# Optimization experiments

Hardware: AMD Instinct MI355X
Metric: run time of the kernel (lower is better)

The kernel has to match this reference:

```python
import jax, jax.numpy as jnp
import numpy as np

D_MODEL = 1024
D_STATE = 128
D_CONV = 4
EXPAND = 2
HEADDIM = 64
NGROUPS = 1
CHUNK = 256
D_INNER = EXPAND * D_MODEL          # 2048
NHEADS = D_INNER // HEADDIM         # 32
D_IN_PROJ = 2 * D_INNER + 2 * NGROUPS * D_STATE + NHEADS  # 4384
CONV_DIM = D_INNER + 2 * NGROUPS * D_STATE                # 2304
BATCH, SEQLEN = 2, 2048


def rmsnorm(x, w, eps=1e-6):
    ms = jnp.mean(x * x, axis=-1, keepdims=True)
    return w * (x * jax.lax.rsqrt(ms + eps))


def layernorm(x, eps=1e-5):
    mu = jnp.mean(x, axis=-1, keepdims=True)
    var = jnp.mean((x - mu) ** 2, axis=-1, keepdims=True)
    return (x - mu) * jax.lax.rsqrt(var + eps)


def activation_quant(x):
    # int8-style fake quant with STE, scale differentiable (matches torch)
    amax = jnp.clip(jnp.max(jnp.abs(x), axis=-1, keepdims=True), 1e-5, None)
    scale = 127.0 / amax
    q = jnp.clip(jnp.round(x * scale), -128, 127)
    return (jax.lax.stop_gradient(q - x * scale) + x * scale) / scale


def weight_quant(w):
    # ternary {-1,0,1}; note: NOT rescaled by scale (matches the triton kernel)
    scale = jnp.clip(jnp.mean(jnp.abs(w)), 1e-5, None)
    wq = jnp.clip(jnp.round(w / scale), -1.0, 1.0)
    return w + jax.lax.stop_gradient(wq - w)  # STE: identity grad


def bitlinear(x, w):
    return activation_quant(layernorm(x)) @ weight_quant(w).T


def segsum(x):
    # x: [..., T] -> [..., T, T] lower-triangular cumulative segment sums
    T = x.shape[-1]
    cs = jnp.cumsum(x, axis=-1)
    ss = cs[..., :, None] - cs[..., None, :]
    mask = jnp.tril(jnp.ones((T, T), dtype=bool))
    return jnp.where(mask, ss, -jnp.inf)


def ssd(u, a, B, C, chunk):
    # u: b l h p (= x*dt); a: b l h (= A*dt); B, C: b l h n (per-head)
    b, l, h, p = u.shape
    n = B.shape[-1]
    c = l // chunk
    u = u.reshape(b, c, chunk, h, p)
    a = a.reshape(b, c, chunk, h).transpose(0, 3, 1, 2)   # b h c s
    B = B.reshape(b, c, chunk, h, n)
    C = C.reshape(b, c, chunk, h, n)
    a_cs = jnp.cumsum(a, axis=-1)                          # b h c s
    L = jnp.exp(segsum(a))                                 # b h c s s
    Y_diag = jnp.einsum('bclhn,bcshn,bhcls,bcshp->bclhp', C, B, L, u)
    decay_states = jnp.exp(a_cs[..., -1:] - a_cs)          # b h c s
    states = jnp.einsum('bclhn,bhcl,bclhp->bchpn', B, decay_states, u)
    a_chunk = jnp.pad(a_cs[..., -1], ((0, 0), (0, 0), (1, 0)))  # b h (c+1)
    decay_chunk = jnp.exp(segsum(a_chunk))                 # b h (c+1) (c+1)
    states = jnp.concatenate([jnp.zeros_like(states[:, :1]), states], axis=1)
    new_states = jnp.einsum('bhzc,bchpn->bzhpn', decay_chunk, states)
    prev_states = new_states[:, :-1]                       # state entering each chunk
    Y_off = jnp.einsum('bclhn,bchpn,bhcl->bclhp', C, prev_states, jnp.exp(a_cs))
    return (Y_diag + Y_off).reshape(b, l, h, p)


def setup_inputs() -> dict:
    key = jax.random.key(0)
    ks = jax.random.split(key, 6)
    hidden_states = jax.random.normal(ks[0], (BATCH, SEQLEN, D_MODEL), jnp.float32)
    in_proj_w = jax.random.normal(ks[1], (D_IN_PROJ, D_MODEL), jnp.float32) / np.sqrt(D_MODEL).astype(np.float32)
    out_proj_w = jax.random.normal(ks[2], (D_MODEL, D_INNER), jnp.float32) / np.sqrt(D_INNER).astype(np.float32)
    conv_w = jax.random.normal(ks[3], (CONV_DIM, D_CONV), jnp.float32) * 0.1
    conv_b = jnp.zeros((CONV_DIM,), jnp.float32)
    A_log = jnp.log(jnp.arange(1, NHEADS + 1, dtype=jnp.float32))
    Dp = jnp.ones((NHEADS,), jnp.float32)
    dt_min, dt_max, dt_floor = 1e-3, 1e-1, 1e-4
    inv_dt = jnp.exp(jax.random.uniform(ks[4], (NHEADS,)) * (np.log(dt_max) - np.log(dt_min)) + np.log(dt_min))
    inv_dt = jnp.clip(inv_dt, dt_floor, None)
    dt_bias = inv_dt + jnp.log(-jnp.expm1(-inv_dt))
    norm_w = jnp.ones((D_MODEL,), jnp.float32)
    out_norm_w = jnp.ones((D_INNER,), jnp.float32)
    return dict(hidden_states=hidden_states, norm_w=norm_w, in_proj_w=in_proj_w,
                conv_w=conv_w, conv_b=conv_b, A_log=A_log, Dp=Dp, dt_bias=dt_bias,
                out_norm_w=out_norm_w, out_proj_w=out_proj_w)


def reference(hidden_states, norm_w, in_proj_w, conv_w, conv_b, A_log, Dp, dt_bias, out_norm_w, out_proj_w):
    b, l, _ = hidden_states.shape
    h = rmsnorm(hidden_states, norm_w)
    zxbcdt = bitlinear(h, in_proj_w)                       # b l (2*d_inner + 2*g*n + h)
    z = zxbcdt[..., :D_INNER]
    xBC = zxbcdt[..., D_INNER:D_INNER + CONV_DIM]
    dt = zxbcdt[..., D_INNER + CONV_DIM:]                  # b l h
    # causal depthwise conv1d (kernel D_CONV) + silu
    xp = jnp.pad(xBC, ((0, 0), (D_CONV - 1, 0), (0, 0)))
    conv = sum(xp[:, k:k + l, :] * conv_w[:, k] for k in range(D_CONV)) + conv_b
    xBC = jax.nn.silu(conv)
    x = xBC[..., :D_INNER].reshape(b, l, NHEADS, HEADDIM)
    Bm = xBC[..., D_INNER:D_INNER + NGROUPS * D_STATE].reshape(b, l, NGROUPS, D_STATE)
    Cm = xBC[..., D_INNER + NGROUPS * D_STATE:].reshape(b, l, NGROUPS, D_STATE)
    hpg = NHEADS // NGROUPS
    Bh = jnp.repeat(Bm, hpg, axis=2)                       # b l h n
    Ch = jnp.repeat(Cm, hpg, axis=2)
    dt = jax.nn.softplus(dt + dt_bias)                     # dt_softplus=True
    A = -jnp.exp(A_log)
    y = ssd(x * dt[..., None], dt * A, Bh, Ch, CHUNK)      # b l h p
    y = y + x * Dp[None, None, :, None]                    # D skip
    y = y * jax.nn.silu(z).reshape(b, l, NHEADS, HEADDIM)  # z gate
    y = rmsnorm(y.reshape(b, l, D_INNER), out_norm_w)
    out = bitlinear(y, out_proj_w)
    return hidden_states + out
```

## Files before the change

kernel.cpp:

```cpp
#include <hip/hip_runtime.h>
#include <stdint.h>
#include <stddef.h>
#include <math.h>

#define TOKS 4096
#define DM   1024
#define DIP  4384
#define DI   2048
#define CVD  2304
#define NH   32
#define HD   64
#define DST  128
#define NCH  8
#define CHK  256

typedef int v4i  __attribute__((ext_vector_type(4)));
typedef int v16i __attribute__((ext_vector_type(16)));
typedef short s8v __attribute__((ext_vector_type(8)));
typedef float f16v __attribute__((ext_vector_type(16)));
typedef unsigned short ushort_t;

static const size_t OFF_ZX    = 0;
static const size_t OFF_SX    = OFF_ZX + (size_t)TOKS*DIP*4;
static const size_t OFF_ST    = OFF_SX + (size_t)TOKS*CVD*4;
static const size_t OFF_YG    = OFF_ST + (size_t)512*HD*DST*4;
static const size_t OFF_Q1    = OFF_YG + (size_t)TOKS*DI*4;
static const size_t OFF_Q2    = OFF_Q1 + (size_t)TOKS*DM;
static const size_t OFF_WQ1   = OFF_Q2 + (size_t)TOKS*DI;
static const size_t OFF_WQ2   = OFF_WQ1 + (size_t)DIP*DM;
static const size_t OFF_RS1   = OFF_WQ2 + (size_t)DM*DI;
static const size_t OFF_RS2   = OFF_RS1 + (size_t)TOKS*4;
static const size_t OFF_DT    = OFF_RS2 + (size_t)TOKS*4;
static const size_t OFF_ACS   = OFF_DT + (size_t)TOKS*NH*4;
static const size_t OFF_CSUM  = OFF_ACS + (size_t)512*CHK*8;
static const size_t OFF_PART  = OFF_CSUM + 512*8;
static const size_t OFF_WSC   = OFF_PART + 1024*8;
static const size_t OFF_BH    = OFF_WSC + 64;
static const size_t OFF_BL    = OFF_BH  + (size_t)TOKS*128*2;
static const size_t OFF_CHG   = OFF_BL  + (size_t)TOKS*128*2;
static const size_t OFF_CLG   = OFF_CHG + (size_t)TOKS*128*2;
static const size_t OFF_GRAM  = OFF_CLG + (size_t)TOKS*128*2;
static const size_t OFF_UTH   = OFF_GRAM + (size_t)16*256*256*4;
static const size_t OFF_UTL   = OFF_UTH + (size_t)512*64*256*2;
static const size_t OFF_PH    = OFF_UTL + (size_t)512*64*256*2;
static const size_t OFF_PL    = OFF_PH  + (size_t)512*64*128*2;

__device__ __forceinline__ ushort_t f2bf(float x) {
  union { float f; unsigned int u; } v; v.f = x;
  unsigned int r = v.u + 0x7FFFu + ((v.u >> 16) & 1u);
  return (ushort_t)(r >> 16);
}
__device__ __forceinline__ float bf2f(ushort_t h) {
  union { unsigned int u; float f; } v; v.u = ((unsigned int)h) << 16;
  return v.f;
}

__device__ __forceinline__ double bsumd(double v, double* sb) {
#pragma unroll
  for (int o = 32; o; o >>= 1) v += __shfl_down(v, o);
  int lane = threadIdx.x & 63, w = threadIdx.x >> 6;
  __syncthreads();
  if (lane == 0) sb[w] = v;
  __syncthreads();
  return sb[0] + sb[1] + sb[2] + sb[3];
}
__device__ __forceinline__ double bmaxd(double v, double* sb) {
#pragma unroll
  for (int o = 32; o; o >>= 1) v = fmax(v, __shfl_down(v, o));
  int lane = threadIdx.x & 63, w = threadIdx.x >> 6;
  __syncthreads();
  if (lane == 0) sb[w] = v;
  __syncthreads();
  return fmax(fmax(sb[0], sb[1]), fmax(sb[2], sb[3]));
}

__global__ void __launch_bounds__(256) k_absmean(const float* __restrict__ w, int n, double* __restrict__ part) {
  double s = 0.0;
  for (int i = blockIdx.x * 256 + threadIdx.x; i < n; i += 512 * 256) s += (double)fabsf(w[i]);
  __shared__ double sb[4];
  s = bsumd(s, sb);
  if (threadIdx.x == 0) part[blockIdx.x] = s;
}

__global__ void __launch_bounds__(256) k_wscale(const double* __restrict__ part, double* __restrict__ wsc, int n1, int n2) {
  __shared__ double sb[4];
  double s = part[threadIdx.x] + part[threadIdx.x + 256];
  double t1 = bsumd(s, sb);
  __syncthreads();
  s = part[512 + threadIdx.x] + part[512 + threadIdx.x + 256];
  double t2 = bsumd(s, sb);
  if (threadIdx.x == 0) {
    wsc[0] = fmax(t1 / (double)n1, 1e-5);
    wsc[1] = fmax(t2 / (double)n2, 1e-5);
  }
}

__global__ void __launch_bounds__(256) k_tern(const float* __restrict__ w, int n, const double* __restrict__ wsc, int which, int8_t* __restrict__ out) {
  int i = blockIdx.x * 256 + threadIdx.x;
  if (i < n) {
    double sc = wsc[which];
    double q = fmin(fmax(rint((double)w[i] / sc), -1.0), 1.0);
    out[i] = (int8_t)q;
  }
}

template <int D>
__global__ void __launch_bounds__(256) k_normquant(const float* __restrict__ in, const float* __restrict__ w,
                                                   int8_t* __restrict__ q, float* __restrict__ rs) {
  constexpr int E = D / 256;
  int t = blockIdx.x, tid = threadIdx.x;
  const float* row = in + (size_t)t * D;
  __shared__ double sb[4];
  double x[E];
  double ss = 0.0;
#pragma unroll
  for (int i = 0; i < E; i++) { x[i] = (double)row[tid + 256 * i]; ss += x[i] * x[i]; }
  ss = bsumd(ss, sb);
  double rr = 1.0 / sqrt(ss / (double)D + 1e-6);
  double s1 = 0.0;
#pragma unroll
  for (int i = 0; i < E; i++) { x[i] = (double)w[tid + 256 * i] * (x[i] * rr); s1 += x[i]; }
  s1 = bsumd(s1, sb);
  double mu = s1 / (double)D;
  double s2 = 0.0;
#pragma unroll
  for (int i = 0; i < E; i++) { double d = x[i] - mu; s2 += d * d; }
  s2 = bsumd(s2, sb);
  double rv = 1.0 / sqrt(s2 / (double)D + 1e-5);
  double am = 0.0;
#pragma unroll
  for (int i = 0; i < E; i++) { x[i] = (x[i] - mu) * rv; am = fmax(am, fabs(x[i])); }
  am = bmaxd(am, sb);
  am = fmax(am, 1e-5);
  double sc = 127.0 / am;
#pragma unroll
  for (int i = 0; i < E; i++) {
    double qq = fmin(fmax(rint(x[i] * sc), -128.0), 127.0);
    q[(size_t)t * D + tid + 256 * i] = (int8_t)qq;
  }
  if (tid == 0) rs[t] = (float)(am / 127.0);
}

__global__ void __launch_bounds__(256, 3) k_gemm_mfma(const int8_t* __restrict__ A, const int8_t* __restrict__ W,
                                                      const float* __restrict__ rs, const float* __restrict__ addend,
                                                      float* __restrict__ out, int M, int N, int K) {
  __shared__ int8_t Al[128 * 80];
  __shared__ int8_t Bl[128 * 80];
  int m0 = blockIdx.x * 128, n0 = blockIdx.y * 128;
  int t = threadIdx.x;
  int w = t >> 6, lane = t & 63;
  int wm = w >> 1, wn = w & 1;
  int l31 = lane & 31, lh = lane >> 5;

  v16i acc[2][2] = {};

  for (int k0 = 0; k0 < K; k0 += 64) {
    __syncthreads();
#pragma unroll
    for (int it = 0; it < 2; ++it) {
      int c = t + 256 * it;
      int row = c >> 2, kc = (c & 3) * 16;
      int4 av = *(const int4*)(A + (size_t)(m0 + row) * K + k0 + kc);
      *(int4*)(Al + row * 80 + kc) = av;
      int4 bv;
      if (n0 + row < N) bv = *(const int4*)(W + (size_t)(n0 + row) * K + k0 + kc);
      else { bv.x = bv.y = bv.z = bv.w = 0; }
      *(int4*)(Bl + row * 80 + kc) = bv;
    }
    __syncthreads();
#pragma unroll
    for (int ks = 0; ks < 2; ++ks) {
      v4i af[2], bf[2];
#pragma unroll
      for (int tm = 0; tm < 2; ++tm)
        af[tm] = *(const v4i*)(Al + (wm * 64 + tm * 32 + l31) * 80 + ks * 32 + lh * 16);
#pragma unroll
      for (int tn = 0; tn < 2; ++tn)
        bf[tn] = *(const v4i*)(Bl + (wn * 64 + tn * 32 + l31) * 80 + ks * 32 + lh * 16);
#pragma unroll
      for (int tm = 0; tm < 2; ++tm)
#pragma unroll
        for (int tn = 0; tn < 2; ++tn)
          acc[tm][tn] = __builtin_amdgcn_mfma_i32_32x32x32_i8(af[tm], bf[tn], acc[tm][tn], 0, 0, 0);
    }
  }

#pragma unroll
  for (int tm = 0; tm < 2; ++tm)
#pragma unroll
    for (int tn = 0; tn < 2; ++tn) {
      int n = n0 + wn * 64 + tn * 32 + l31;
      if (n < N) {
#pragma unroll
        for (int r = 0; r < 16; ++r) {
          int mrel = (r & 3) + 8 * (r >> 2) + 4 * lh;
          int m = m0 + wm * 64 + tm * 32 + mrel;
          float v = rs[m] * (float)acc[tm][tn][r];
          if (addend) v += addend[(size_t)m * N + n];
          out[(size_t)m * N + n] = v;
        }
      }
    }
}

__global__ void __launch_bounds__(256) k_conv(const float* __restrict__ zx, const float* __restrict__ cw,
                                              const float* __restrict__ cb, float* __restrict__ sx) {
  int c = blockIdx.x * 256 + threadIdx.x;
  int t = blockIdx.y;
  int b = t >> 11, l = t & 2047;
  float acc = cb[c];
#pragma unroll
  for (int k = 0; k < 4; k++) {
    int li = l - 3 + k;
    if (li >= 0) acc = fmaf(zx[(size_t)(b * 2048 + li) * DIP + DI + c], cw[c * 4 + k], acc);
  }
  sx[(size_t)t * CVD + c] = acc / (1.f + expf(-acc));
}

__global__ void __launch_bounds__(256) k_splitbc(const float* __restrict__ sx,
                                                 ushort_t* __restrict__ bh, ushort_t* __restrict__ bl,
                                                 ushort_t* __restrict__ ch, ushort_t* __restrict__ cl) {
  int idx = blockIdx.x * 256 + threadIdx.x;
  int tok = idx >> 6, c4 = (idx & 63) * 4;
  float4 v = *(const float4*)(sx + (size_t)tok * CVD + DI + c4);
  float f[4] = {v.x, v.y, v.z, v.w};
  ushort_t hh[4], ll[4];
#pragma unroll
  for (int j = 0; j < 4; j++) { hh[j] = f2bf(f[j]); ll[j] = f2bf(f[j] - bf2f(hh[j])); }
  uint2 hv, lv;
  hv.x = (unsigned)hh[0] | ((unsigned)hh[1] << 16); hv.y = (unsigned)hh[2] | ((unsigned)hh[3] << 16);
  lv.x = (unsigned)ll[0] | ((unsigned)ll[1] << 16); lv.y = (unsigned)ll[2] | ((unsigned)ll[3] << 16);
  if (c4 < 128) {
    *(uint2*)(bh + (size_t)tok * 128 + c4) = hv;
    *(uint2*)(bl + (size_t)tok * 128 + c4) = lv;
  } else {
    *(uint2*)(ch + (size_t)tok * 128 + c4 - 128) = hv;
    *(uint2*)(cl + (size_t)tok * 128 + c4 - 128) = lv;
  }
}

__global__ void __launch_bounds__(256) k_dt(const float* __restrict__ zx, const float* __restrict__ dt_bias,
                                            float* __restrict__ dtv) {
  int idx = blockIdx.x * 256 + threadIdx.x;
  int t = idx >> 5, h = idx & 31;
  float x = zx[(size_t)t * DIP + (DI + CVD) + h] + dt_bias[h];
  dtv[idx] = fmaxf(x, 0.f) + log1pf(expf(-fabsf(x)));
}

__global__ void __launch_bounds__(256) k_cumsum(const float* __restrict__ dtv, const float* __restrict__ A_log,
                                                double* __restrict__ acs, double* __restrict__ csum) {
  int bid = blockIdx.x;
  int h = bid & 31, bc = bid >> 5;
  int s = threadIdx.x;
  int tok = bc * 256 + s;
  double negA = -exp((double)A_log[h]);
  double a = (double)dtv[tok * 32 + h] * negA;
  __shared__ double buf[256];
  buf[s] = a;
  __syncthreads();
  for (int o = 1; o < 256; o <<= 1) {
    double add = (s >= o) ? buf[s - o] : 0.0;
    __syncthreads();
    buf[s] += add;
    __syncthreads();
  }
  acs[(size_t)bid * 256 + s] = buf[s];
  if (s == 255) csum[bid] = buf[s];
}

__global__ void __launch_bounds__(256) k_gram(const ushort_t* __restrict__ bhg, const ushort_t* __restrict__ blg,
                                              const ushort_t* __restrict__ chg, const ushort_t* __restrict__ clg,
                                              float* __restrict__ gram) {
  int blk = blockIdx.x;
  int bc = blk >> 3, lt = blk & 7;
  int t = threadIdx.x;
  int w = t >> 6, lane = t & 63;
  int l31 = lane & 31, lhf = lane >> 5;
  __shared__ float Gl[4][32 * 36];

  s8v ch[8], cl[8];
  size_t tokA = (size_t)(bc * 256 + lt * 32 + l31) * 128;
#pragma unroll
  for (int ks = 0; ks < 8; ++ks) {
    ch[ks] = *(const s8v*)(chg + tokA + ks * 16 + lhf * 8);
    cl[ks] = *(const s8v*)(clg + tokA + ks * 16 + lhf * 8);
  }
  for (int st = w; st <= lt; st += 4) {
    size_t tokB = (size_t)(bc * 256 + st * 32 + l31) * 128;
    f16v acc = {};
#pragma unroll
    for (int ks = 0; ks < 8; ++ks) {
      s8v bh = *(const s8v*)(bhg + tokB + ks * 16 + lhf * 8);
      s8v bl = *(const s8v*)(blg + tokB + ks * 16 + lhf * 8);
      acc = __builtin_amdgcn_mfma_f32_32x32x16_bf16(ch[ks], bh, acc, 0, 0, 0);
      acc = __builtin_amdgcn_mfma_f32_32x32x16_bf16(ch[ks], bl, acc, 0, 0, 0);
      acc = __builtin_amdgcn_mfma_f32_32x32x16_bf16(cl[ks], bh, acc, 0, 0, 0);
    }
#pragma unroll
    for (int rr = 0; rr < 16; ++rr) {
      int lrow = (rr & 3) + 8 * (rr >> 2) + 4 * lhf;
      Gl[w][lrow * 36 + l31] = acc[rr];
    }
    int lr = lane >> 1, c0 = (lane & 1) * 16;
    float* gdst = gram + ((size_t)bc * 256 + lt * 32 + lr) * 256 + st * 32 + c0;
#pragma unroll
    for (int i = 0; i < 4; ++i)
      *(float4*)(gdst + i * 4) = *(const float4*)(&Gl[w][lr * 36 + c0 + i * 4]);
  }
}

__global__ void __launch_bounds__(256) k_prepuT(const float* __restrict__ sx, const float* __restrict__ dtv,
                                                ushort_t* __restrict__ uth, ushort_t* __restrict__ utl) {
  int r = blockIdx.x;
  int h = r & 31, bc = r >> 5;
  int t = threadIdx.x;
  __shared__ float Xs[64 * 68];
  __shared__ float dts[64];
  for (int slab = 0; slab < 4; ++slab) {
    int s0 = slab * 64;
    if (slab) __syncthreads();
    if (t < 64) dts[t] = dtv[(size_t)(bc * 256 + s0 + t) * 32 + h];
    {
      int s = t >> 2, pg = (t & 3) * 16;
      const float* xr = sx + (size_t)(bc * 256 + s0 + s) * CVD + h * 64 + pg;
      float* dst = &Xs[s * 68 + pg];
#pragma unroll
      for (int i = 0; i < 4; ++i)
        *(float4*)(dst + i * 4) = *(const float4*)(xr + i * 4);
    }
    __syncthreads();
    {
      int p = t >> 2, sg = (t & 3) * 16;
      union { int4 q[2]; ushort_t e[16]; } H, L;
#pragma unroll
      for (int j = 0; j < 16; ++j) {
        float f = Xs[(sg + j) * 68 + p] * dts[sg + j];
        ushort_t hh = f2bf(f);
        H.e[j] = hh;
        L.e[j] = f2bf(f - bf2f(hh));
      }
      size_t base = ((size_t)r * 64 + p) * 256 + s0 + sg;
      *(int4*)(uth + base) = H.q[0];
      *(int4*)(uth + base + 8) = H.q[1];
      *(int4*)(utl + base) = L.q[0];
      *(int4*)(utl + base + 8) = L.q[1];
    }
  }
}

__global__ void __launch_bounds__(256, 4) k_states2(const float* __restrict__ sx, const float* __restrict__ dtv,
                                                    const double* __restrict__ acs, const double* __restrict__ csum,
                                                    float* __restrict__ states) {
  int r = blockIdx.x;
  int h = r & 31, bc = r >> 5;
  int t = threadIdx.x, tx = t & 15, ty = t >> 4;
  __shared__ float du[64 * 68];
  double last = csum[r];
  float acc[4][8] = {};
  for (int s0 = 0; s0 < 256; s0 += 64) {
    __syncthreads();
    {
      int s = t >> 2, pg = (t & 3) * 16;
      int tok = bc * 256 + s0 + s;
      float w = expf((float)(last - acs[(size_t)r * 256 + s0 + s])) * dtv[(size_t)tok * 32 + h];
      const float* xr = sx + (size_t)tok * CVD + h * 64 + pg;
      float* dst = &du[s * 68 + pg];
#pragma unroll
      for (int i = 0; i < 4; i++) {
        float4 v = *(const float4*)(xr + i * 4);
        v.x *= w; v.y *= w; v.z *= w; v.w *= w;
        *(float4*)(dst + i * 4) = v;
      }
    }
    __syncthreads();
#pragma unroll 4
    for (int s = 0; s < 64; s++) {
      int tok = bc * 256 + s0 + s;
      const float* br = sx + (size_t)tok * CVD + DI + ty * 8;
      float4 b0 = *(const float4*)(br);
      float4 b1 = *(const float4*)(br + 4);
      float4 d4 = *(const float4*)(&du[s * 68 + tx * 4]);
      float dd[4] = {d4.x, d4.y, d4.z, d4.w};
      float bv[8] = {b0.x, b0.y, b0.z, b0.w, b1.x, b1.y, b1.z, b1.w};
#pragma unroll
      for (int i = 0; i < 4; i++)
#pragma unroll
        for (int j = 0; j < 8; j++) acc[i][j] = fmaf(dd[i], bv[j], acc[i][j]);
    }
  }
  size_t base = (size_t)r * (HD * DST);
#pragma unroll
  for (int i = 0; i < 4; i++) {
    float4 v0, v1;
    v0.x = acc[i][0]; v0.y = acc[i][1]; v0.z = acc[i][2]; v0.w = acc[i][3];
    v1.x = acc[i][4]; v1.y = acc[i][5]; v1.z = acc[i][6]; v1.w = acc[i][7];
    *(float4*)(states + base + (size_t)(tx * 4 + i) * DST + ty * 8) = v0;
    *(float4*)(states + base + (size_t)(tx * 4 + i) * DST + ty * 8 + 4) = v1;
  }
}

__global__ void __launch_bounds__(256) k_chunkscan(float* __restrict__ states, const double* __restrict__ csum,
                                                   ushort_t* __restrict__ ph, ushort_t* __restrict__ pl) {
  int idx = blockIdx.x * 256 + threadIdx.x;
  int n = idx & 127, p = (idx >> 7) & 63, h = (idx >> 13) & 31, b = idx >> 18;
  float Nv = 0.f;
  for (int c = 0; c < 8; c++) {
    int bid = (b * 8 + c) * 32 + h;
    size_t addr = (size_t)bid * (HD * DST) + p * DST + n;
    float s = states[addr];
    states[addr] = Nv;
    ushort_t hh = f2bf(Nv);
    ph[addr] = hh;
    pl[addr] = f2bf(Nv - bf2f(hh));
    Nv = Nv * expf((float)csum[bid]) + s;
  }
}

__global__ void __launch_bounds__(256) k_y6(const float* __restrict__ sx, const double* __restrict__ acs,
                                            const ushort_t* __restrict__ chg, const ushort_t* __restrict__ clg,
                                            const ushort_t* __restrict__ prevh, const ushort_t* __restrict__ prevl,
                                            const float* __restrict__ gram,
                                            const ushort_t* __restrict__ uth, const ushort_t* __restrict__ utl,
                                            const float* __restrict__ zx, const float* __restrict__ Dp,
                                            float* __restrict__ yg) {
  int bid = blockIdx.x;
  int r = bid >> 1, half = bid & 1;
  int h = r & 31, bc = r >> 5;
  int t = threadIdx.x;
  int w = t >> 6, lane = t & 63;
  int l31 = lane & 31, lhf = lane >> 5;
  int lw = half * 128 + w * 32;
  int lg = lw + l31;

  __shared__ ushort_t Uh[2][64 * 36], Ul[2][64 * 36];
  __shared__ double acs_s[256];
  acs_s[t] = acs[(size_t)r * 256 + t];

  int nsub = half * 4 + 4;
  {
    int p = t >> 2, sg = (t & 3) * 8;
    size_t gb = ((size_t)r * 64 + p) * 256 + sg;
    const uint2* s1 = (const uint2*)(uth + gb);
    uint2* d1 = (uint2*)(&Uh[0][p * 36 + sg]);
    d1[0] = s1[0]; d1[1] = s1[1];
    const uint2* s2 = (const uint2*)(utl + gb);
    uint2* d2 = (uint2*)(&Ul[0][p * 36 + sg]);
    d2[0] = s2[0]; d2[1] = s2[1];
  }
  __syncthreads();

  f16v Yacc[2] = {};
  {
    size_t ca = (size_t)(bc * 256 + lg) * 128;
#pragma unroll
    for (int ks = 0; ks < 8; ++ks) {
      s8v ch = *(const s8v*)(chg + ca + ks * 16 + lhf * 8);
      s8v cl = *(const s8v*)(clg + ca + ks * 16 + lhf * 8);
#pragma unroll
      for (int pt = 0; pt < 2; ++pt) {
        size_t pa = ((size_t)r * 64 + pt * 32 + l31) * 128 + ks * 16 + lhf * 8;
        s8v ph = *(const s8v*)(prevh + pa);
        s8v pl = *(const s8v*)(prevl + pa);
        Yacc[pt] = __builtin_amdgcn_mfma_f32_32x32x16_bf16(ch, ph, Yacc[pt], 0, 0, 0);
        Yacc[pt] = __builtin_amdgcn_mfma_f32_32x32x16_bf16(ch, pl, Yacc[pt], 0, 0, 0);
        Yacc[pt] = __builtin_amdgcn_mfma_f32_32x32x16_bf16(cl, ph, Yacc[pt], 0, 0, 0);
      }
    }
  }
#pragma unroll
  for (int rr = 0; rr < 16; ++rr) {
    int lrow = (rr & 3) + 8 * (rr >> 2) + 4 * lhf;
    float el = expf((float)acs_s[lw + lrow]);
    Yacc[0][rr] *= el;
    Yacc[1][rr] *= el;
  }

  for (int st = 0; st < nsub; ++st) {
    int s0 = st * 32, cur = st & 1;
    if (st + 1 < nsub) {
      int p = t >> 2, sg = (t & 3) * 8;
      int nb = cur ^ 1;
      size_t gb = ((size_t)r * 64 + p) * 256 + s0 + 32 + sg;
      const uint2* s1 = (const uint2*)(uth + gb);
      uint2* d1 = (uint2*)(&Uh[nb][p * 36 + sg]);
      d1[0] = s1[0]; d1[1] = s1[1];
      const uint2* s2 = (const uint2*)(utl + gb);
      uint2* d2 = (uint2*)(&Ul[nb][p * 36 + sg]);
      d2[0] = s2[0]; d2[1] = s2[1];
    }
    if (s0 <= lw + 31) {
      double a_l = acs_s[lg];
      const float* gp = gram + ((size_t)(bc * 256 + lg)) * 256 + s0;
#pragma unroll
      for (int ks2 = 0; ks2 < 2; ++ks2) {
        int kb = ks2 * 16 + lhf * 8;
        float4 g0 = *(const float4*)(gp + kb);
        float4 g1 = *(const float4*)(gp + kb + 4);
        float gv[8] = {g0.x, g0.y, g0.z, g0.w, g1.x, g1.y, g1.z, g1.w};
        union { s8v v; ushort_t e[8]; } AH, AL;
#pragma unroll
        for (int j = 0; j < 8; ++j) {
          int s = s0 + kb + j;
          float v = 0.f;
          if (s <= lg) v = expf((float)(a_l - acs_s[s])) * gv[j];
          ushort_t hh = f2bf(v);
          AH.e[j] = hh;
          AL.e[j] = f2bf(v - bf2f(hh));
        }
#pragma unroll
        for (int pt = 0; pt < 2; ++pt) {
          union { s8v v; uint2 d[2]; } uh, ul;
          int ub = (pt * 32 + l31) * 36 + kb;
          uh.d[0] = *(const uint2*)(&Uh[cur][ub]);
          uh.d[1] = *(const uint2*)(&Uh[cur][ub + 4]);
          ul.d[0] = *(const uint2*)(&Ul[cur][ub]);
          ul.d[1] = *(const uint2*)(&Ul[cur][ub + 4]);
          Yacc[pt] = __builtin_amdgcn_mfma_f32_32x32x16_bf16(AH.v, uh.v, Yacc[pt], 0, 0, 0);
          Yacc[pt] = __builtin_amdgcn_mfma_f32_32x32x16_bf16(AH.v, ul.v, Yacc[pt], 0, 0, 0);
          Yacc[pt] = __builtin_amdgcn_mfma_f32_32x32x16_bf16(AL.v, uh.v, Yacc[pt], 0, 0, 0);
        }
      }
    }
    __syncthreads();
  }

  float dph = Dp[h];
#pragma unroll
  for (int pt = 0; pt < 2; ++pt) {
    int p = pt * 32 + l31;
#pragma unroll
    for (int rr = 0; rr < 16; ++rr) {
      int lrow = (rr & 3) + 8 * (rr >> 2) + 4 * lhf;
      size_t tok = (size_t)(bc * 256 + lw + lrow);
      float xv = sx[tok * CVD + h * 64 + p];
      float zv = zx[tok * DIP + h * 64 + p];
      float y = (Yacc[pt][rr] + xv * dph) * (zv / (1.f + expf(-zv)));
      yg[tok * DI + h * 64 + p] = y;
    }
  }
}

extern "C" void kernel_launch(void* const* d_in, const int* in_sizes, int n_in,
                              void* d_out, int out_size, void* d_ws, size_t ws_size,
                              hipStream_t stream) {
  const float* hidden   = (const float*)d_in[0];
  const float* norm_w   = (const float*)d_in[1];
  const float* in_proj  = (const float*)d_in[2];
  const float* conv_w   = (const float*)d_in[3];
  const float* conv_b   = (const float*)d_in[4];
  const float* A_log    = (const float*)d_in[5];
  const float* Dp       = (const float*)d_in[6];
  const float* dt_bias  = (const float*)d_in[7];
  const float* out_norm = (const float*)d_in[8];
  const float* out_proj = (const float*)d_in[9];
  float* out = (float*)d_out;

  char* ws = (char*)d_ws;
  float*  zx    = (float*)(ws + OFF_ZX);
  float*  sx    = (float*)(ws + OFF_SX);
  float*  st    = (float*)(ws + OFF_ST);
  float*  yg    = (float*)(ws + OFF_YG);
  int8_t* q1    = (int8_t*)(ws + OFF_Q1);
  int8_t* q2    = (int8_t*)(ws + OFF_Q2);
  int8_t* wq1   = (int8_t*)(ws + OFF_WQ1);
  int8_t* wq2   = (int8_t*)(ws + OFF_WQ2);
  float*  rs1   = (float*)(ws + OFF_RS1);
  float*  rs2   = (float*)(ws + OFF_RS2);
  float*  dtv   = (float*)(ws + OFF_DT);
  double* acs   = (double*)(ws + OFF_ACS);
  double* csum  = (double*)(ws + OFF_CSUM);
  double* part  = (double*)(ws + OFF_PART);
  double* wsc   = (double*)(ws + OFF_WSC);
  ushort_t* bhg = (ushort_t*)(ws + OFF_BH);
  ushort_t* blg = (ushort_t*)(ws + OFF_BL);
  ushort_t* chg = (ushort_t*)(ws + OFF_CHG);
  ushort_t* clg = (ushort_t*)(ws + OFF_CLG);
  float*  gram  = (float*)(ws + OFF_GRAM);
  ushort_t* uth = (ushort_t*)(ws + OFF_UTH);
  ushort_t* utl = (ushort_t*)(ws + OFF_UTL);
  ushort_t* pvh = (ushort_t*)(ws + OFF_PH);
  ushort_t* pvl = (ushort_t*)(ws + OFF_PL);

  const int n1 = DIP * DM, n2 = DM * DI;

  hipLaunchKernelGGL(k_absmean, dim3(512), dim3(256), 0, stream, in_proj, n1, part);
  hipLaunchKernelGGL(k_absmean, dim3(512), dim3(256), 0, stream, out_proj, n2, part + 512);
  hipLaunchKernelGGL(k_wscale, dim3(1), dim3(256), 0, stream, part, wsc, n1, n2);
  hipLaunchKernelGGL(k_tern, dim3((n1 + 255) / 256), dim3(256), 0, stream, in_proj, n1, wsc, 0, wq1);
  hipLaunchKernelGGL(k_tern, dim3((n2 + 255) / 256), dim3(256), 0, stream, out_proj, n2, wsc, 1, wq2);
  hipLaunchKernelGGL(k_normquant<DM>, dim3(TOKS), dim3(256), 0, stream, hidden, norm_w, q1, rs1);
  hipLaunchKernelGGL(k_gemm_mfma, dim3(TOKS / 128, (DIP + 127) / 128), dim3(256), 0, stream,
                     q1, wq1, rs1, (const float*)nullptr, zx, TOKS, DIP, DM);
  hipLaunchKernelGGL(k_conv, dim3(CVD / 256, TOKS), dim3(256), 0, stream, zx, conv_w, conv_b, sx);
  hipLaunchKernelGGL(k_splitbc, dim3(TOKS * 64 / 256), dim3(256), 0, stream, sx, bhg, blg, chg, clg);
  hipLaunchKernelGGL(k_dt, dim3(TOKS * NH / 256), dim3(256), 0, stream, zx, dt_bias, dtv);
  hipLaunchKernelGGL(k_cumsum, dim3(512), dim3(256), 0, stream, dtv, A_log, acs, csum);
  hipLaunchKernelGGL(k_gram, dim3(128), dim3(256), 0, stream, bhg, blg, chg, clg, gram);
  hipLaunchKernelGGL(k_prepuT, dim3(512), dim3(256), 0, stream, sx, dtv, uth, utl);
  hipLaunchKernelGGL(k_states2, dim3(512), dim3(256), 0, stream, sx, dtv, acs, csum, st);
  hipLaunchKernelGGL(k_chunkscan, dim3(2 * NH * HD * DST / 256), dim3(256), 0, stream, st, csum, pvh, pvl);
  hipLaunchKernelGGL(k_y6, dim3(1024), dim3(256), 0, stream, sx, acs, chg, clg, pvh, pvl, gram, uth, utl, zx, Dp, yg);
  hipLaunchKernelGGL(k_normquant<DI>, dim3(TOKS), dim3(256), 0, stream, yg, out_norm, q2, rs2);
  hipLaunchKernelGGL(k_gemm_mfma, dim3(TOKS / 128, DM / 128), dim3(256), 0, stream,
                     q2, wq2, rs2, hidden, out, TOKS, DM, DI);
  (void)in_sizes; (void)n_in; (void)out_size; (void)ws_size;
}
```

Baseline: 388.9 us.

## Split Y kernel into single-wave blocks with per-wave causal loop bounds

Replaces the 256-thread k_y6 block, which shared a double-buffered LDS tile of U across four waves, with k_y7, a 64-thread single-wave kernel over 4096 blocks. Each wave loops only over the causal sub-tiles it needs (st <= lt), so there is no per-block barrier and no idle waves on the triangular part. U and acs are now read straight from global memory instead of being staged in LDS. Block IDs are swizzled so neighbouring blocks land on different row groups. The trade-off is more global and L2 traffic for U, plus the loss of LDS reuse between waves.

```diff
diff --git a/kernel.cpp b/kernel.cpp
--- a/kernel.cpp
+++ b/kernel.cpp
@@ -416,38 +416,22 @@
   }
 }
 
-__global__ void __launch_bounds__(256) k_y6(const float* __restrict__ sx, const double* __restrict__ acs,
-                                            const ushort_t* __restrict__ chg, const ushort_t* __restrict__ clg,
-                                            const ushort_t* __restrict__ prevh, const ushort_t* __restrict__ prevl,
-                                            const float* __restrict__ gram,
-                                            const ushort_t* __restrict__ uth, const ushort_t* __restrict__ utl,
-                                            const float* __restrict__ zx, const float* __restrict__ Dp,
-                                            float* __restrict__ yg) {
-  int bid = blockIdx.x;
-  int r = bid >> 1, half = bid & 1;
+__global__ void __launch_bounds__(64) k_y7(const float* __restrict__ sx, const double* __restrict__ acs,
+                                           const ushort_t* __restrict__ chg, const ushort_t* __restrict__ clg,
+                                           const ushort_t* __restrict__ prevh, const ushort_t* __restrict__ prevl,
+                                           const float* __restrict__ gram,
+                                           const ushort_t* __restrict__ uth, const ushort_t* __restrict__ utl,
+                                           const float* __restrict__ zx, const float* __restrict__ Dp,
+                                           float* __restrict__ yg) {
+  int myid = (blockIdx.x & 7) * 512 + (blockIdx.x >> 3);
+  int r = myid >> 3, lt = myid & 7;
   int h = r & 31, bc = r >> 5;
-  int t = threadIdx.x;
-  int w = t >> 6, lane = t & 63;
+  int lane = threadIdx.x;
   int l31 = lane & 31, lhf = lane >> 5;
-  int lw = half * 128 + w * 32;
+  int lw = lt * 32;
   int lg = lw + l31;
-
-  __shared__ ushort_t Uh[2][64 * 36], Ul[2][64 * 36];
-  __shared__ double acs_s[256];
-  acs_s[t] = acs[(size_t)r * 256 + t];
-
-  int nsub = half * 4 + 4;
-  {
-    int p = t >> 2, sg = (t & 3) * 8;
-    size_t gb = ((size_t)r * 64 + p) * 256 + sg;
-    const uint2* s1 = (const uint2*)(uth + gb);
-    uint2* d1 = (uint2*)(&Uh[0][p * 36 + sg]);
-    d1[0] = s1[0]; d1[1] = s1[1];
-    const uint2* s2 = (const uint2*)(utl + gb);
-    uint2* d2 = (uint2*)(&Ul[0][p * 36 + sg]);
-    d2[0] = s2[0]; d2[1] = s2[1];
-  }
-  __syncthreads();
+  const double* acsr = acs + (size_t)r * 256;
+  double a_l = acsr[lg];
 
   f16v Yacc[2] = {};
   {
@@ -470,58 +454,40 @@
 #pragma unroll
   for (int rr = 0; rr < 16; ++rr) {
     int lrow = (rr & 3) + 8 * (rr >> 2) + 4 * lhf;
-    float el = expf((float)acs_s[lw + lrow]);
+    float el = expf((float)acsr[lw + lrow]);
     Yacc[0][rr] *= el;
     Yacc[1][rr] *= el;
   }
 
-  for (int st = 0; st < nsub; ++st) {
-    int s0 = st * 32, cur = st & 1;
-    if (st + 1 < nsub) {
-      int p = t >> 2, sg = (t & 3) * 8;
-      int nb = cur ^ 1;
-      size_t gb = ((size_t)r * 64 + p) * 256 + s0 + 32 + sg;
-      const uint2* s1 = (const uint2*)(uth + gb);
-      uint2* d1 = (uint2*)(&Uh[nb][p * 36 + sg]);
-      d1[0] = s1[0]; d1[1] = s1[1];
-      const uint2* s2 = (const uint2*)(utl + gb);
-      uint2* d2 = (uint2*)(&Ul[nb][p * 36 + sg]);
-      d2[0] = s2[0]; d2[1] = s2[1];
-    }
-    if (s0 <= lw + 31) {
-      double a_l = acs_s[lg];
-      const float* gp = gram + ((size_t)(bc * 256 + lg)) * 256 + s0;
-#pragma unroll
-      for (int ks2 = 0; ks2 < 2; ++ks2) {
-        int kb = ks2 * 16 + lhf * 8;
-        float4 g0 = *(const float4*)(gp + kb);
-        float4 g1 = *(const float4*)(gp + kb + 4);
-        float gv[8] = {g0.x, g0.y, g0.z, g0.w, g1.x, g1.y, g1.z, g1.w};
-        union { s8v v; ushort_t e[8]; } AH, AL;
-#pragma unroll
-        for (int j = 0; j < 8; ++j) {
-          int s = s0 + kb + j;
-          float v = 0.f;
-          if (s <= lg) v = expf((float)(a_l - acs_s[s])) * gv[j];
-          ushort_t hh = f2bf(v);
-          AH.e[j] = hh;
-          AL.e[j] = f2bf(v - bf2f(hh));
-        }
-#pragma unroll
-        for (int pt = 0; pt < 2; ++pt) {
-          union { s8v v; uint2 d[2]; } uh, ul;
-          int ub = (pt * 32 + l31) * 36 + kb;
-          uh.d[0] = *(const uint2*)(&Uh[cur][ub]);
-          uh.d[1] = *(const uint2*)(&Uh[cur][ub + 4]);
-          ul.d[0] = *(const uint2*)(&Ul[cur][ub]);
-          ul.d[1] = *(const uint2*)(&Ul[cur][ub + 4]);
-          Yacc[pt] = __builtin_amdgcn_mfma_f32_32x32x16_bf16(AH.v, uh.v, Yacc[pt], 0, 0, 0);
-          Yacc[pt] = __builtin_amdgcn_mfma_f32_32x32x16_bf16(AH.v, ul.v, Yacc[pt], 0, 0, 0);
-          Yacc[pt] = __builtin_amdgcn_mfma_f32_32x32x16_bf16(AL.v, uh.v, Yacc[pt], 0, 0, 0);
-        }
+  for (int st = 0; st <= lt; ++st) {
+    int s0 = st * 32;
+    const float* gp = gram + (size_t)(bc * 256 + lg) * 256 + s0;
+#pragma unroll
+    for (int ks2 = 0; ks2 < 2; ++ks2) {
+      int kb = ks2 * 16 + lhf * 8;
+      float4 g0 = *(const float4*)(gp + kb);
+      float4 g1 = *(const float4*)(gp + kb + 4);
+      float gv[8] = {g0.x, g0.y, g0.z, g0.w, g1.x, g1.y, g1.z, g1.w};
+      union { s8v v; ushort_t e[8]; } AH, AL;
+#pragma unroll
+      for (int j = 0; j < 8; ++j) {
+        int s = s0 + kb + j;
+        float v = 0.f;
+        if (s <= lg) v = expf((float)(a_l - acsr[s])) * gv[j];
+        ushort_t hh = f2bf(v);
+        AH.e[j] = hh;
+        AL.e[j] = f2bf(v - bf2f(hh));
       }
-    }
-    __syncthreads();
+#pragma unroll
+      for (int pt = 0; pt < 2; ++pt) {
+        size_t ub = ((size_t)r * 64 + pt * 32 + l31) * 256 + s0 + kb;
+        s8v uh = *(const s8v*)(uth + ub);
+        s8v ul = *(const s8v*)(utl + ub);
+        Yacc[pt] = __builtin_amdgcn_mfma_f32_32x32x16_bf16(AH.v, uh, Yacc[pt], 0, 0, 0);
+        Yacc[pt] = __builtin_amdgcn_mfma_f32_32x32x16_bf16(AH.v, ul, Yacc[pt], 0, 0, 0);
+        Yacc[pt] = __builtin_amdgcn_mfma_f32_32x32x16_bf16(AL.v, uh, Yacc[pt], 0, 0, 0);
+      }
+    }
   }
 
   float dph = Dp[h];
@@ -599,7 +565,7 @@
   hipLaunchKernelGGL(k_prepuT, dim3(512), dim3(256), 0, stream, sx, dtv, uth, utl);
   hipLaunchKernelGGL(k_states2, dim3(512), dim3(256), 0, stream, sx, dtv, acs, csum, st);
   hipLaunchKernelGGL(k_chunkscan, dim3(2 * NH * HD * DST / 256), dim3(256), 0, stream, st, csum, pvh, pvl);
-  hipLaunchKernelGGL(k_y6, dim3(1024), dim3(256), 0, stream, sx, acs, chg, clg, pvh, pvl, gram, uth, utl, zx, Dp, yg);
+  hipLaunchKernelGGL(k_y7, dim3(4096), dim3(64), 0, stream, sx, acs, chg, clg, pvh, pvl, gram, uth, utl, zx, Dp, yg);
   hipLaunchKernelGGL(k_normquant<DI>, dim3(TOKS), dim3(256), 0, stream, yg, out_norm, q2, rs2);
   hipLaunchKernelGGL(k_gemm_mfma, dim3(TOKS / 128, DM / 128), dim3(256), 0, stream,
                      q2, wq2, rs2, hidden, out, TOKS, DM, DI);
```

Result: slower. 419.2 us (+7.8%).
